# Kernel tuning notes

Hardware: AMD Instinct MI355X
Metric: run time of the kernel (lower is better)

The kernel has to match this reference:

```python
import jax, jax.numpy as jnp
import numpy as np

WS, SS, NH = 7, 3, 4  # window_size, shift_size, num_heads


def _rel_position_index(wh, ww):
    # torch doublestepseq: seq1 step (2*Ww-1) len Wh, seq2 step 1 len Ww
    seq1 = np.arange(wh) * (2 * ww - 1)
    seq2 = np.arange(ww)
    rel = (seq1[:, None] + seq2[None, :]).reshape(1, -1)  # [1, Wh*Ww]
    idx = rel + rel.T                                      # [N, N]
    return np.ascontiguousarray(idx[:, ::-1])              # flip dim 1


def _shift_mask(hp, wp, ws, ss):
    img = np.zeros((hp, wp))
    cnt = 0
    sls = (slice(0, -ws), slice(-ws, -ss), slice(-ss, None))
    for h in sls:
        for w in sls:
            img[h, w] = cnt
            cnt += 1
    mw = img.reshape(hp // ws, ws, wp // ws, ws).transpose(0, 2, 1, 3).reshape(-1, ws * ws)
    diff = mw[:, None, :] - mw[:, :, None]  # [nW, N, N]
    return np.where(diff != 0, -100.0, 0.0).astype(np.float32)


def setup_inputs() -> dict:
    key = jax.random.key(0)
    ks = jax.random.split(key, 6)
    B, H, W, C = 64, 56, 56, 128
    return {
        "query": jax.random.normal(ks[0], (B, H * W, C), jnp.float32),
        "rpb_table": jax.random.normal(ks[1], ((2 * WS - 1) ** 2, NH), jnp.float32) * 0.02,
        "qkv_w": jax.random.normal(ks[2], (3 * C, C), jnp.float32) * (C ** -0.5),
        "qkv_b": jax.random.normal(ks[3], (3 * C,), jnp.float32) * 0.02,
        "proj_w": jax.random.normal(ks[4], (C, C), jnp.float32) * (C ** -0.5),
        "proj_b": jax.random.normal(ks[5], (C,), jnp.float32) * 0.02,
        "H": H,
        "W": W,
    }


def reference(query, rpb_table, qkv_w, qkv_b, proj_w, proj_b, H, W):
    B, L, C = query.shape
    hd = C // NH
    N = WS * WS
    x = query.reshape(B, H, W, C)
    pad_b, pad_r = (-H) % WS, (-W) % WS
    x = jnp.pad(x, ((0, 0), (0, pad_b), (0, pad_r), (0, 0)))
    Hp, Wp = H + pad_b, W + pad_r
    nW = (Hp // WS) * (Wp // WS)
    # cyclic shift
    x = jnp.roll(x, (-SS, -SS), axis=(1, 2))
    # window partition -> [B*nW, N, C]
    xw = x.reshape(B, Hp // WS, WS, Wp // WS, WS, C).transpose(0, 1, 3, 2, 4, 5).reshape(-1, N, C)
    nB = xw.shape[0]
    qkv = (xw @ qkv_w.T + qkv_b).reshape(nB, N, 3, NH, hd).transpose(2, 0, 3, 1, 4)
    q, k, v = qkv[0] * (hd ** -0.5), qkv[1], qkv[2]
    attn = jnp.einsum("bhnd,bhmd->bhnm", q, k)  # [nB, NH, N, N]
    rel_idx = _rel_position_index(WS, WS)
    bias = rpb_table[rel_idx.reshape(-1)].reshape(N, N, NH).transpose(2, 0, 1)
    attn = attn + bias[None]
    mask = jnp.asarray(_shift_mask(Hp, Wp, WS, SS))  # [nW, N, N]
    attn = (attn.reshape(B, nW, NH, N, N) + mask[None, :, None]).reshape(nB, NH, N, N)
    attn = jax.nn.softmax(attn, axis=-1)
    out = jnp.einsum("bhnm,bhmd->bhnd", attn, v).transpose(0, 2, 1, 3).reshape(nB, N, C)
    out = out @ proj_w.T + proj_b
    # window reverse
    out = out.reshape(B, Hp // WS, Wp // WS, WS, WS, C).transpose(0, 1, 3, 2, 4, 5).reshape(B, Hp, Wp, C)
    out = jnp.roll(out, (SS, SS), axis=(1, 2))[:, :H, :W, :]
    return out.reshape(B, H * W, C)
```

## Files before the change

kernel.cpp:

```cpp
#include <hip/hip_runtime.h>

typedef short s16x8 __attribute__((ext_vector_type(8)));
typedef short s16x4 __attribute__((ext_vector_type(4)));
typedef float f32x4 __attribute__((ext_vector_type(4)));
typedef unsigned short u16;

namespace {

constexpr int NHEAD = 4;
constexpr int CDIM  = 128;
constexpr int NTOK  = 49;
constexpr int IMG   = 56;
constexpr int NWIN  = 4096;
constexpr float QSCALE = 0.17677669529663687f;

__device__ inline u16 f2bf(float x) {
  unsigned u = __float_as_uint(x);
  u += 0x7fffu + ((u >> 16) & 1u);
  return (u16)(u >> 16);
}
__device__ inline float bf2f(u16 h) { return __uint_as_float(((unsigned)h) << 16); }
__device__ inline int div7(int t) { return (t * 9363) >> 16; }

__device__ inline f32x4 mfma32(s16x8 a, s16x8 b, f32x4 c) {
  return __builtin_amdgcn_mfma_f32_16x16x32_bf16(a, b, c, 0, 0, 0);
}
__device__ inline f32x4 mfma16(s16x4 a, s16x4 b, f32x4 c) {
#if __has_builtin(__builtin_amdgcn_mfma_f32_16x16x16bf16_1k)
  return __builtin_amdgcn_mfma_f32_16x16x16bf16_1k(a, b, c, 0, 0, 0);
#else
  f32x4 d;
  asm volatile("v_mfma_f32_16x16x16_bf16 %0, %1, %2, %3"
               : "=v"(d) : "v"(a), "v"(b), "v"(c));
  return d;
#endif
}
__device__ inline s16x4 pack4(f32x4 v) {
  s16x4 r;
  r[0] = (short)f2bf(v[0]); r[1] = (short)f2bf(v[1]);
  r[2] = (short)f2bf(v[2]); r[3] = (short)f2bf(v[3]);
  return r;
}

__global__ void prep(const float* __restrict__ qkvw, const float* __restrict__ projw,
                     const float* __restrict__ rpb,
                     u16* __restrict__ wq, u16* __restrict__ wp, u16* __restrict__ btab) {
  int i = blockIdx.x * 256 + threadIdx.x;
  if (i < 384 * 128) wq[i] = f2bf(qkvw[i]);
  if (i < 128 * 128) wp[i] = f2bf(projw[i]);
  if (i < 65536) {
    int m = i & 63, n = (i >> 6) & 63, h = (i >> 12) & 3, cls = (i >> 14) & 3;
    float v;
    if (m >= NTOK) v = -1e9f;
    else if (n >= NTOK) v = 0.f;
    else {
      int tin = div7(n), tjn = n - tin * 7;
      int tim = div7(m), tjm = m - tim * 7;
      int ridx = 13 * (tin - tim + 6) + (tjn - tjm + 6);
      v = rpb[ridx * NHEAD + h];
      int wy = (cls & 2) ? 7 : 0, wx = (cls & 1) ? 7 : 0;
      int mhn = wy * 7 + tin, mwn = wx * 7 + tjn;
      int mhm = wy * 7 + tim, mwm = wx * 7 + tjm;
      int cn = ((mhn < 49) ? 0 : ((mhn < 53) ? 1 : 2)) * 3 + ((mwn < 49) ? 0 : ((mwn < 53) ? 1 : 2));
      int cm = ((mhm < 49) ? 0 : ((mhm < 53) ? 1 : 2)) * 3 + ((mwm < 49) ? 0 : ((mwm < 53) ? 1 : 2));
      if (cn != cm) v -= 100.f;
    }
    btab[i] = f2bf(v);
  }
}

__device__ inline int adr128(int r, int c) {
  return r * 128 + (c & 7) + 8 * (((c >> 3) ^ (r & 7)) & 15);
}

__global__ __launch_bounds__(64) void swin_wave(
    const float* __restrict__ xin,
    const float* __restrict__ qkvb,
    const float* __restrict__ projb,
    const u16*  __restrict__ wq,
    const u16*  __restrict__ wp,
    const u16*  __restrict__ btab,
    float* __restrict__ outp)
{
  __shared__ u16 o_lds[8192];

  const int wb = blockIdx.x;
  const int bb = wb >> 6, wy = (wb >> 3) & 7, wx = wb & 7;
  const int lane = threadIdx.x;
  const int g = lane >> 4, lj = lane & 15;
  const int cls = ((wy == 7) ? 2 : 0) | ((wx == 7) ? 1 : 0);

  auto gposf = [&](int tok) -> int {
    int t  = (tok < NTOK) ? tok : 0;
    int ti = div7(t), tj = t - ti * 7;
    int gh = wy * 7 + ti + 3; if (gh >= IMG) gh -= IMG;
    int gw = wx * 7 + tj + 3; if (gw >= IMG) gw -= IMG;
    return gh * IMG + gw;
  };

  const float* xb = xin + (size_t)bb * (IMG * IMG * CDIM);
  s16x8 X[4][4];
  #pragma unroll
  for (int mt = 0; mt < 4; ++mt) {
    int tok = 16 * mt + lj;
    bool ok = tok < NTOK;
    const float* xr = xb + (size_t)gposf(tok) * CDIM;
    #pragma unroll
    for (int ks = 0; ks < 4; ++ks) {
      s16x8 r = {0, 0, 0, 0, 0, 0, 0, 0};
      if (ok) {
        float4 a = *reinterpret_cast<const float4*>(xr + 32 * ks + 8 * g);
        float4 b = *reinterpret_cast<const float4*>(xr + 32 * ks + 8 * g + 4);
        r[0] = (short)f2bf(a.x); r[1] = (short)f2bf(a.y);
        r[2] = (short)f2bf(a.z); r[3] = (short)f2bf(a.w);
        r[4] = (short)f2bf(b.x); r[5] = (short)f2bf(b.y);
        r[6] = (short)f2bf(b.z); r[7] = (short)f2bf(b.w);
      }
      X[mt][ks] = r;
    }
  }

  #pragma unroll 1
  for (int h = 0; h < NHEAD; ++h) {
    s16x4 Kbf[4][2];
    #pragma unroll
    for (int dt = 0; dt < 2; ++dt) {
      s16x8 wa[4];
      #pragma unroll
      for (int ks = 0; ks < 4; ++ks)
        wa[ks] = *reinterpret_cast<const s16x8*>(
            &wq[(size_t)(128 + 32 * h + 16 * dt + lj) * 128 + 32 * ks + 8 * g]);
      f32x4 bk4 = *reinterpret_cast<const f32x4*>(&qkvb[128 + 32 * h + 16 * dt + 4 * g]);
      #pragma unroll
      for (int mt = 0; mt < 4; ++mt) {
        f32x4 c = {0.f, 0.f, 0.f, 0.f};
        #pragma unroll
        for (int ks = 0; ks < 4; ++ks) c = mfma32(wa[ks], X[mt][ks], c);
        Kbf[mt][dt] = pack4(c + bk4);
      }
    }
    s16x4 Qbf[2][4];
    #pragma unroll
    for (int dt = 0; dt < 2; ++dt) {
      s16x8 wa[4];
      #pragma unroll
      for (int ks = 0; ks < 4; ++ks)
        wa[ks] = *reinterpret_cast<const s16x8*>(
            &wq[(size_t)(32 * h + 16 * dt + lj) * 128 + 32 * ks + 8 * g]);
      f32x4 bq4 = *reinterpret_cast<const f32x4*>(&qkvb[32 * h + 16 * dt + 4 * g]);
      #pragma unroll
      for (int nt = 0; nt < 4; ++nt) {
        f32x4 c = {0.f, 0.f, 0.f, 0.f};
        #pragma unroll
        for (int ks = 0; ks < 4; ++ks) c = mfma32(wa[ks], X[nt][ks], c);
        f32x4 q;
        #pragma unroll
        for (int r2 = 0; r2 < 4; ++r2) q[r2] = (c[r2] + bq4[r2]) * QSCALE;
        Qbf[dt][nt] = pack4(q);
      }
    }
    s16x4 Vbf[4][2];
    #pragma unroll
    for (int dt = 0; dt < 2; ++dt) {
      s16x8 wbv[4];
      #pragma unroll
      for (int ks = 0; ks < 4; ++ks)
        wbv[ks] = *reinterpret_cast<const s16x8*>(
            &wq[(size_t)(256 + 32 * h + 16 * dt + lj) * 128 + 32 * ks + 8 * g]);
      float bv = qkvb[256 + 32 * h + 16 * dt + lj];
      #pragma unroll
      for (int mt = 0; mt < 4; ++mt) {
        f32x4 c = {0.f, 0.f, 0.f, 0.f};
        #pragma unroll
        for (int ks = 0; ks < 4; ++ks) c = mfma32(X[mt][ks], wbv[ks], c);
        f32x4 v;
        #pragma unroll
        for (int r2 = 0; r2 < 4; ++r2) v[r2] = c[r2] + bv;
        Vbf[mt][dt] = pack4(v);
      }
    }
    const u16* bt = btab + (((cls << 2) + h) << 12);
    s16x4 Pt[4][4];
    #pragma unroll
    for (int nt = 0; nt < 4; ++nt) {
      f32x4 st[4];
      #pragma unroll
      for (int mt = 0; mt < 4; ++mt) {
        f32x4 c = mfma16(Kbf[mt][0], Qbf[0][nt], (f32x4){0.f, 0.f, 0.f, 0.f});
        c = mfma16(Kbf[mt][1], Qbf[1][nt], c);
        s16x4 bb4 = *reinterpret_cast<const s16x4*>(&bt[((16 * nt + lj) << 6) + 16 * mt + 4 * g]);
        #pragma unroll
        for (int r2 = 0; r2 < 4; ++r2) c[r2] += bf2f((u16)bb4[r2]);
        st[mt] = c;
      }
      float mx = -3e38f;
      #pragma unroll
      for (int mt = 0; mt < 4; ++mt)
        #pragma unroll
        for (int r2 = 0; r2 < 4; ++r2) mx = fmaxf(mx, st[mt][r2]);
      mx = fmaxf(mx, __shfl_xor(mx, 16, 64));
      mx = fmaxf(mx, __shfl_xor(mx, 32, 64));
      float sm = 0.f;
      #pragma unroll
      for (int mt = 0; mt < 4; ++mt)
        #pragma unroll
        for (int r2 = 0; r2 < 4; ++r2) {
          float e = __expf(st[mt][r2] - mx);
          st[mt][r2] = e;
          sm += e;
        }
      sm += __shfl_xor(sm, 16, 64);
      sm += __shfl_xor(sm, 32, 64);
      float inv = 1.f / sm;
      #pragma unroll
      for (int mt = 0; mt < 4; ++mt) {
        f32x4 p;
        #pragma unroll
        for (int r2 = 0; r2 < 4; ++r2) p[r2] = st[mt][r2] * inv;
        Pt[mt][nt] = pack4(p);
      }
    }
    #pragma unroll
    for (int dt = 0; dt < 2; ++dt)
      #pragma unroll
      for (int nt = 0; nt < 4; ++nt) {
        f32x4 oc = {0.f, 0.f, 0.f, 0.f};
        #pragma unroll
        for (int mt = 0; mt < 4; ++mt) oc = mfma16(Vbf[mt][dt], Pt[mt][nt], oc);
        s16x4 ov = pack4(oc);
        *reinterpret_cast<s16x4*>(&o_lds[adr128(16 * nt + lj, 32 * h + 16 * dt + 4 * g)]) = ov;
      }
  }

  float* ob = outp + (size_t)bb * (IMG * IMG * CDIM);
  #pragma unroll 1
  for (int nt = 0; nt < 4; ++nt) {
    s16x4 oa[8];
    #pragma unroll
    for (int kp = 0; kp < 8; ++kp)
      oa[kp] = *reinterpret_cast<const s16x4*>(&o_lds[adr128(16 * nt + lj, 16 * kp + 4 * g)]);
    int gp[4];
    #pragma unroll
    for (int r2 = 0; r2 < 4; ++r2) gp[r2] = gposf(16 * nt + 4 * g + r2);
    #pragma unroll
    for (int ct = 0; ct < 8; ++ct) {
      f32x4 y = {0.f, 0.f, 0.f, 0.f};
      #pragma unroll
      for (int kp = 0; kp < 8; ++kp) {
        s16x4 wpb = *reinterpret_cast<const s16x4*>(
            &wp[(size_t)(16 * ct + lj) * 128 + 16 * kp + 4 * g]);
        y = mfma16(oa[kp], wpb, y);
      }
      float bias = projb[16 * ct + lj];
      #pragma unroll
      for (int r2 = 0; r2 < 4; ++r2) {
        int tok = 16 * nt + 4 * g + r2;
        if (tok < NTOK)
          ob[(size_t)gp[r2] * CDIM + 16 * ct + lj] = y[r2] + bias;
      }
    }
  }
}

}

extern "C" void kernel_launch(void* const* d_in, const int* in_sizes, int n_in,
                              void* d_out, int out_size, void* d_ws, size_t ws_size,
                              hipStream_t stream) {
  const float* x     = (const float*)d_in[0];
  const float* rpb   = (const float*)d_in[1];
  const float* qkvw  = (const float*)d_in[2];
  const float* qkvb  = (const float*)d_in[3];
  const float* projw = (const float*)d_in[4];
  const float* projb = (const float*)d_in[5];
  u16* wq   = (u16*)d_ws;
  u16* wp   = wq + 384 * 128;
  u16* btab = wp + 128 * 128;

  prep<<<256, 256, 0, stream>>>(qkvw, projw, rpb, wq, wp, btab);
  swin_wave<<<NWIN, 64, 0, stream>>>(x, qkvb, projb, wq, wp, btab, (float*)d_out);
}
```

Before: 150.5 us.

## Keep attention output in registers and reorder projection loop over output tiles

Drops the shared-memory staging buffer for per-head attention output and keeps all 32 output fragments in registers, with the head loop fully unrolled. The projection loop is inverted so each weight tile is loaded once and reused across the four token tiles, cutting repeated weight loads. Launch bounds now request two blocks per CU, and the float-to-bf16 conversion uses the HIP intrinsic. The aim is to remove LDS round-trips and redundant global weight reads, at the cost of much higher register pressure that could cause spills.

```diff
diff --git a/kernel.cpp b/kernel.cpp
--- a/kernel.cpp
+++ b/kernel.cpp
@@ -1,4 +1,5 @@
 #include <hip/hip_runtime.h>
+#include <hip/hip_bf16.h>
 
 typedef short s16x8 __attribute__((ext_vector_type(8)));
 typedef short s16x4 __attribute__((ext_vector_type(4)));
@@ -15,9 +16,9 @@
 constexpr float QSCALE = 0.17677669529663687f;
 
 __device__ inline u16 f2bf(float x) {
-  unsigned u = __float_as_uint(x);
-  u += 0x7fffu + ((u >> 16) & 1u);
-  return (u16)(u >> 16);
+  union { __hip_bfloat16 b; u16 u; } cv;
+  cv.b = __float2bfloat16(x);
+  return cv.u;
 }
 __device__ inline float bf2f(u16 h) { return __uint_as_float(((unsigned)h) << 16); }
 __device__ inline int div7(int t) { return (t * 9363) >> 16; }
@@ -69,11 +70,7 @@
   }
 }
 
-__device__ inline int adr128(int r, int c) {
-  return r * 128 + (c & 7) + 8 * (((c >> 3) ^ (r & 7)) & 15);
-}
-
-__global__ __launch_bounds__(64) void swin_wave(
+__global__ __launch_bounds__(64, 2) void swin_wave(
     const float* __restrict__ xin,
     const float* __restrict__ qkvb,
     const float* __restrict__ projb,
@@ -82,8 +79,6 @@
     const u16*  __restrict__ btab,
     float* __restrict__ outp)
 {
-  __shared__ u16 o_lds[8192];
-
   const int wb = blockIdx.x;
   const int bb = wb >> 6, wy = (wb >> 3) & 7, wx = wb & 7;
   const int lane = threadIdx.x;
@@ -120,7 +115,9 @@
     }
   }
 
-  #pragma unroll 1
+  s16x4 oa[4][8];
+
+  #pragma unroll
   for (int h = 0; h < NHEAD; ++h) {
     s16x4 Kbf[4][2];
     #pragma unroll
@@ -180,7 +177,6 @@
       }
     }
     const u16* bt = btab + (((cls << 2) + h) << 12);
-    s16x4 Pt[4][4];
     #pragma unroll
     for (int nt = 0; nt < 4; ++nt) {
       f32x4 st[4];
@@ -212,52 +208,52 @@
       sm += __shfl_xor(sm, 16, 64);
       sm += __shfl_xor(sm, 32, 64);
       float inv = 1.f / sm;
+      s16x4 Pt[4];
       #pragma unroll
       for (int mt = 0; mt < 4; ++mt) {
         f32x4 p;
         #pragma unroll
         for (int r2 = 0; r2 < 4; ++r2) p[r2] = st[mt][r2] * inv;
-        Pt[mt][nt] = pack4(p);
-      }
-    }
-    #pragma unroll
-    for (int dt = 0; dt < 2; ++dt)
-      #pragma unroll
-      for (int nt = 0; nt < 4; ++nt) {
+        Pt[mt] = pack4(p);
+      }
+      #pragma unroll
+      for (int dt = 0; dt < 2; ++dt) {
         f32x4 oc = {0.f, 0.f, 0.f, 0.f};
         #pragma unroll
-        for (int mt = 0; mt < 4; ++mt) oc = mfma16(Vbf[mt][dt], Pt[mt][nt], oc);
-        s16x4 ov = pack4(oc);
-        *reinterpret_cast<s16x4*>(&o_lds[adr128(16 * nt + lj, 32 * h + 16 * dt + 4 * g)]) = ov;
-      }
-  }
-
+        for (int mt = 0; mt < 4; ++mt) oc = mfma16(Vbf[mt][dt], Pt[mt], oc);
+        oa[nt][2 * h + dt] = pack4(oc);
+      }
+    }
+  }
+
+  int gp[4][4];
+  bool tv[4][4];
+  #pragma unroll
+  for (int nt = 0; nt < 4; ++nt)
+    #pragma unroll
+    for (int r2 = 0; r2 < 4; ++r2) {
+      int tok = 16 * nt + 4 * g + r2;
+      gp[nt][r2] = gposf(tok);
+      tv[nt][r2] = tok < NTOK;
+    }
   float* ob = outp + (size_t)bb * (IMG * IMG * CDIM);
   #pragma unroll 1
-  for (int nt = 0; nt < 4; ++nt) {
-    s16x4 oa[8];
+  for (int ct = 0; ct < 8; ++ct) {
+    s16x4 wpb[8];
     #pragma unroll
     for (int kp = 0; kp < 8; ++kp)
-      oa[kp] = *reinterpret_cast<const s16x4*>(&o_lds[adr128(16 * nt + lj, 16 * kp + 4 * g)]);
-    int gp[4];
-    #pragma unroll
-    for (int r2 = 0; r2 < 4; ++r2) gp[r2] = gposf(16 * nt + 4 * g + r2);
-    #pragma unroll
-    for (int ct = 0; ct < 8; ++ct) {
+      wpb[kp] = *reinterpret_cast<const s16x4*>(
+          &wp[(size_t)(16 * ct + lj) * 128 + 16 * kp + 4 * g]);
+    float bias = projb[16 * ct + lj];
+    #pragma unroll
+    for (int nt = 0; nt < 4; ++nt) {
       f32x4 y = {0.f, 0.f, 0.f, 0.f};
       #pragma unroll
-      for (int kp = 0; kp < 8; ++kp) {
-        s16x4 wpb = *reinterpret_cast<const s16x4*>(
-            &wp[(size_t)(16 * ct + lj) * 128 + 16 * kp + 4 * g]);
-        y = mfma16(oa[kp], wpb, y);
-      }
-      float bias = projb[16 * ct + lj];
-      #pragma unroll
-      for (int r2 = 0; r2 < 4; ++r2) {
-        int tok = 16 * nt + 4 * g + r2;
-        if (tok < NTOK)
-          ob[(size_t)gp[r2] * CDIM + 16 * ct + lj] = y[r2] + bias;
-      }
+      for (int kp = 0; kp < 8; ++kp) y = mfma16(oa[nt][kp], wpb[kp], y);
+      #pragma unroll
+      for (int r2 = 0; r2 < 4; ++r2)
+        if (tv[nt][r2])
+          ob[(size_t)gp[nt][r2] * CDIM + 16 * ct + lj] = y[r2] + bias;
     }
   }
 }
```

Result: no change. 151.1 us (+0.4%).
